# Kernel optimization log

Measured on AMD Instinct MI355X. Metric: run time of the kernel, lower is better.

## Reference

```python
import jax, jax.numpy as jnp
import numpy as np

DIM = 192
HEADS = 6
WH, WW = 7, 7
N = WH * WW            # 49 tokens per window
NW = 64                # windows per image
B = 64                 # images
B_ = NW * B            # 4096 window-batches
HEAD_DIM = DIM // HEADS
TABLE = (2 * WH - 1) * (2 * WW - 1)  # 169


def _relative_position_index():
    ch, cw = np.meshgrid(np.arange(WH), np.arange(WW), indexing='ij')
    coords = np.stack([ch, cw]).reshape(2, -1)          # (2, N)
    rel = coords[:, :, None] - coords[:, None, :]       # (2, N, N)
    rel = rel.transpose(1, 2, 0).astype(np.int32)
    rel[:, :, 0] += WH - 1
    rel[:, :, 1] += WW - 1
    rel[:, :, 0] *= 2 * WW - 1
    return jnp.asarray(rel.sum(-1))                     # (N, N) int32


def setup_inputs() -> dict:
    key = jax.random.key(0)
    ks = jax.random.split(key, 7)
    x = jax.random.normal(ks[0], (B_, N, DIM), dtype=jnp.float32)
    # 0 / -100 additive window mask (as produced by shifted-window masking)
    m = jax.random.uniform(ks[1], (NW, N, N))
    mask = jnp.where(m < 0.8, 0.0, -100.0).astype(jnp.float32)
    qkv_w = jax.random.normal(ks[2], (3 * DIM, DIM), dtype=jnp.float32) * 0.02
    qkv_b = jnp.zeros((3 * DIM,), dtype=jnp.float32)
    proj_w = jax.random.normal(ks[3], (DIM, DIM), dtype=jnp.float32) * 0.02
    proj_b = jnp.zeros((DIM,), dtype=jnp.float32)
    rpb_table = jax.random.normal(ks[4], (TABLE, HEADS), dtype=jnp.float32) * 0.02
    rel_idx = _relative_position_index()
    return {"x": x, "mask": mask, "qkv_w": qkv_w, "qkv_b": qkv_b,
            "proj_w": proj_w, "proj_b": proj_b, "rpb_table": rpb_table,
            "rel_idx": rel_idx}


def reference(x, mask, qkv_w, qkv_b, proj_w, proj_b, rpb_table, rel_idx):
    Bw, n, c = x.shape
    scale = HEAD_DIM ** -0.5
    qkv = x @ qkv_w.T + qkv_b                                  # (B_, N, 3C)
    qkv = qkv.reshape(Bw, n, 3, HEADS, HEAD_DIM).transpose(2, 0, 3, 1, 4)
    q, k, v = qkv[0], qkv[1], qkv[2]                           # (B_, H, N, hd)
    attn = jnp.einsum('bhid,bhjd->bhij', q * scale, k)          # (B_, H, N, N)
    bias = rpb_table[rel_idx.reshape(-1)].reshape(n, n, HEADS)  # gather
    attn = attn + bias.transpose(2, 0, 1)[None]                 # (1, H, N, N)
    nW = mask.shape[0]
    attn = attn.reshape(Bw // nW, nW, HEADS, n, n) + mask[None, :, None]
    attn = attn.reshape(Bw, HEADS, n, n)
    attn = jax.nn.softmax(attn, axis=-1).astype(v.dtype)
    out = jnp.einsum('bhij,bhjd->bhid', attn, v)                # (B_, H, N, hd)
    out = out.transpose(0, 2, 1, 3).reshape(Bw, n, c)
    return out @ proj_w.T + proj_b
```

## Files before the change

### kernel.cpp

```cpp
#include <hip/hip_runtime.h>

typedef unsigned short u16;
typedef unsigned int   u32;
typedef _Float16 f16x8 __attribute__((ext_vector_type(8)));
typedef __fp16   hf2   __attribute__((ext_vector_type(2)));
typedef float    f32x4 __attribute__((ext_vector_type(4)));

#define NTOK 49
#define CDIM 192
#define NH   6
#define HD   32

#define QOFF   0
#define QSTR   200
#define KOFF   9800
#define VTOFF  19600
#define VTSTR  56
#define XOFF   30352
#define PSTR   72
#define ARENA_U16 40152

#define WS_WQ 0
#define WS_WP 110592
#define WS_BM 147456

static __device__ __forceinline__ u16 f2h(float f){ union{ _Float16 h; u16 u;} v; v.h=(_Float16)f; return v.u; }
static __device__ __forceinline__ u32 pk2(float a, float b){
    hf2 h = __builtin_amdgcn_cvt_pkrtz(a, b);
    return __builtin_bit_cast(u32, h);
}

__global__ void prep_weights(const float* __restrict__ qkv_w,
                             const float* __restrict__ proj_w,
                             u16* __restrict__ ws)
{
    const int idx = blockIdx.x*256 + threadIdx.x;
    if (idx < 110592) {
        const int fid = idx >> 9, r = idx & 511;
        const int lane = r >> 3, e = r & 7;
        const int t = fid/6, k6 = fid - 6*t;
        const int col = t*16 + (lane & 15);
        const int kk  = k6*32 + (lane >> 4)*8 + e;
        ws[WS_WQ + idx] = f2h(qkv_w[col*CDIM + kk]);
    } else if (idx < 147456) {
        const int j = idx - 110592;
        const int fid = j >> 9, r = j & 511;
        const int lane = r >> 3, e = r & 7;
        const int t = fid/6, k6 = fid - 6*t;
        const int col = t*16 + (lane & 15);
        const int kk  = k6*32 + (lane >> 4)*8 + e;
        ws[WS_WP + j] = f2h(proj_w[col*CDIM + kk]);
    }
}

__global__ void prep_bm(const float* __restrict__ mask,
                        const float* __restrict__ rpb,
                        const int*   __restrict__ rel,
                        u16* __restrict__ ws)
{
    const int idx = blockIdx.x*256 + threadIdx.x;
    if (idx >= 64*NH*256*16) return;
    const int r   = idx & 3;
    const int jt  = (idx >> 2) & 3;
    const int tid = (idx >> 4) & 255;
    const int rest = idx >> 12;
    const int h = rest % NH;
    const int w = rest / NH;
    const int i  = 16*(tid >> 6) + (tid & 15);
    const int lg = (tid >> 4) & 3;
    const int j  = jt*16 + 4*lg + r;
    float v;
    if (i >= NTOK)      v = 0.0f;
    else if (j >= NTOK) v = -1e30f;
    else v = rpb[rel[i*NTOK+j]*NH + h] + mask[((size_t)w*NTOK+i)*NTOK + j];
    ws[WS_BM + idx] = f2h(v);
}

#define LDFRAG(B, BASE, t) { const u16* _p = (BASE) + (size_t)(t)*3072 + lane*8;      \
    B[0]=*(const f16x8*)(_p);      B[1]=*(const f16x8*)(_p+512);                      \
    B[2]=*(const f16x8*)(_p+1024); B[3]=*(const f16x8*)(_p+1536);                     \
    B[4]=*(const f16x8*)(_p+2048); B[5]=*(const f16x8*)(_p+2560); }

#define QKV_STEP(s, CUR, NXT, PF) {                                                   \
    if (PF) LDFRAG(NXT, wq, t0+(s)+2);                                                \
    const int _t = t0+(s); const int _sec = _t/12; const int _cb = (_t - _sec*12)*16; \
    f32x4 _ac[4] = {};                                                                \
    if (_sec < 2) {       \
      const float4 _b4 = *(const float4*)&qkv_b[_t*16 + 4*lg];                        \
      _Pragma("unroll") for (int _k=0;_k<6;++_k)                                      \
        _Pragma("unroll") for (int _m=0;_m<4;++_m)                                    \
          _ac[_m] = __builtin_amdgcn_mfma_f32_16x16x32_f16(CUR[_k], A[_k][_m], _ac[_m],0,0,0); \
      const float _sc = (_sec==0) ? 0.17677669529663687f : 1.0f;                      \
      u16* _dst = (_sec==0) ? (arena+QOFF) : (arena+KOFF);                            \
      _Pragma("unroll") for (int _m=0;_m<4;++_m) {                                    \
        const int _tok = 16*_m + l15;                                                 \
        if (_tok < NTOK) {                                                            \
          uint2 _wd = make_uint2(pk2((_ac[_m][0]+_b4.x)*_sc, (_ac[_m][1]+_b4.y)*_sc), \
                                 pk2((_ac[_m][2]+_b4.z)*_sc, (_ac[_m][3]+_b4.w)*_sc));\
          *(uint2*)&_dst[_tok*QSTR + _cb + 4*lg] = _wd; } }                           \
    } else {               \
      const float _b1 = qkv_b[384 + _cb + l15];                                       \
      _Pragma("unroll") for (int _k=0;_k<6;++_k)                                      \
        _Pragma("unroll") for (int _m=0;_m<4;++_m)                                    \
          _ac[_m] = __builtin_amdgcn_mfma_f32_16x16x32_f16(A[_k][_m], CUR[_k], _ac[_m],0,0,0); \
      _Pragma("unroll") for (int _m=0;_m<4;++_m) {                                    \
        if (16*_m + 4*lg <= 48) {                                                     \
          uint2 _wd = make_uint2(pk2(_ac[_m][0]+_b1, _ac[_m][1]+_b1),                 \
                                 pk2(_ac[_m][2]+_b1, _ac[_m][3]+_b1));                \
          *(uint2*)&arena[VTOFF + (_cb + l15)*VTSTR + 16*_m + 4*lg] = _wd; } } } }

#define PROJ_STEP(s, CUR, NXT, PF) {                                                  \
    if (PF) LDFRAG(NXT, wp, p0+(s)+1);                                                \
    f32x4 _ac[4] = {};                                                                \
    _Pragma("unroll") for (int _k=0;_k<6;++_k)                                        \
      _Pragma("unroll") for (int _m=0;_m<4;++_m)                                      \
        _ac[_m] = __builtin_amdgcn_mfma_f32_16x16x32_f16(CUR[_k], PA[_k][_m], _ac[_m],0,0,0); \
    _Pragma("unroll") for (int _m=0;_m<4;++_m) {                                      \
      const int _tok = 16*_m + l15;                                                   \
      if (_tok < NTOK) {                                                              \
        float4 _o = make_float4(_ac[_m][0]+pb4[s].x, _ac[_m][1]+pb4[s].y,             \
                                _ac[_m][2]+pb4[s].z, _ac[_m][3]+pb4[s].w);            \
        *(float4*)&og[(size_t)_tok*CDIM + (p0+(s))*16 + 4*lg] = _o; } } }

__global__ __launch_bounds__(256, 2)
void winattn_core(const float* __restrict__ x,
                  const float* __restrict__ qkv_b,
                  const float* __restrict__ proj_b,
                  const u16* __restrict__ ws,
                  float* __restrict__ out)
{
    __shared__ __align__(16) u16 arena[ARENA_U16];
    const int b    = blockIdx.x;
    const int tid  = threadIdx.x;
    const int lane = tid & 63;
    const int wv   = tid >> 6;
    const int l15  = lane & 15;
    const int lg   = lane >> 4;
    const int win  = b & 63;

    {
        const float4* xg = (const float4*)(x + (size_t)b * (NTOK * CDIM));
        for (int i = tid; i < NTOK * CDIM / 4; i += 256) {
            const float4 v = xg[i];
            const int row = (i * 4) / CDIM, col = (i * 4) % CDIM;
            *(uint2*)&arena[XOFF + row * QSTR + col] =
                make_uint2(pk2(v.x, v.y), pk2(v.z, v.w));
        }
        for (int i = tid; i < CDIM * 7; i += 256)
            arena[VTOFF + (i / 7) * VTSTR + 49 + (i % 7)] = 0;
    }
    __syncthreads();

    const u16* wq = ws + WS_WQ;
    int arow[4];
    #pragma unroll
    for (int m = 0; m < 4; ++m) {
        const int r = 16*m + l15;
        arow[m] = (r < NTOK ? r : NTOK-1) * QSTR;
    }
    const int t0 = wv * 9;
    {
        f16x8 A[6][4];
        #pragma unroll
        for (int k6 = 0; k6 < 6; ++k6)
            #pragma unroll
            for (int m = 0; m < 4; ++m)
                A[k6][m] = *(const f16x8*)&arena[XOFF + arow[m] + k6*32 + 8*lg];
        f16x8 Ba[6], Bb[6], Bc[6];
        LDFRAG(Ba, wq, t0); LDFRAG(Bb, wq, t0+1);
        QKV_STEP(0, Ba, Bc, 1)
        QKV_STEP(1, Bb, Ba, 1)
        QKV_STEP(2, Bc, Bb, 1)
        QKV_STEP(3, Ba, Bc, 1)
        QKV_STEP(4, Bb, Ba, 1)
        QKV_STEP(5, Bc, Bb, 1)
        QKV_STEP(6, Ba, Bc, 1)
        QKV_STEP(7, Bb, Ba, 0)
        QKV_STEP(8, Bc, Bb, 0)
    }

    f16x8 bmf[6][2];
    {
        const u16* bmb = ws + WS_BM + (((size_t)win*NH)*256 + tid)*16;
        #pragma unroll
        for (int h = 0; h < NH; ++h) {
            bmf[h][0] = *(const f16x8*)(bmb + h*4096);
            bmf[h][1] = *(const f16x8*)(bmb + h*4096 + 8);
        }
    }
    __syncthreads();

    const int i0 = 16 * wv;
    const bool myok = (i0 + l15 < NTOK);
    const int myrow = myok ? i0 + l15 : NTOK-1;
    int krow[4];
    #pragma unroll
    for (int jt = 0; jt < 4; ++jt)
        krow[jt] = (jt*16 + l15 < NTOK ? jt*16 + l15 : NTOK-1) * QSTR;

    f16x8 Qf[6];
    #pragma unroll
    for (int h = 0; h < NH; ++h)
        Qf[h] = *(const f16x8*)&arena[QOFF + myrow*QSTR + h*HD + 8*lg];

    #pragma unroll
    for (int h = 0; h < NH; ++h) {
        u16* pp = arena + XOFF + wv*2336 + (h & 1)*1168;
        f32x4 pacc[4];
        #pragma unroll
        for (int jt = 0; jt < 4; ++jt) {
            const f16x8 Kf = *(const f16x8*)&arena[KOFF + krow[jt] + h*HD + 8*lg];
            f32x4 z = {};
            pacc[jt] = __builtin_amdgcn_mfma_f32_16x16x32_f16(Kf, Qf[h], z, 0, 0, 0);
        }
        float val[4][4];
        float mx = -3e38f;
        #pragma unroll
        for (int jt = 0; jt < 4; ++jt)
            #pragma unroll
            for (int r = 0; r < 4; ++r) {
                val[jt][r] = pacc[jt][r] + (float)bmf[h][jt>>1][(jt&1)*4 + r];
                mx = fmaxf(mx, val[jt][r]);
            }
        mx = fmaxf(mx, __shfl_xor(mx, 16));
        mx = fmaxf(mx, __shfl_xor(mx, 32));
        float s = 0.f;
        #pragma unroll
        for (int jt = 0; jt < 4; ++jt)
            #pragma unroll
            for (int r = 0; r < 4; ++r) {
                const float e = __expf(val[jt][r] - mx);
                val[jt][r] = e; s += e;
            }
        s += __shfl_xor(s, 16);
        s += __shfl_xor(s, 32);
        const float inv = 1.0f / s;
        #pragma unroll
        for (int jt = 0; jt < 4; ++jt)
            *(uint2*)&pp[l15*PSTR + jt*16 + 4*lg] =
                make_uint2(pk2(val[jt][0], val[jt][1]), pk2(val[jt][2], val[jt][3]));
        const f16x8 Pb0 = *(const f16x8*)&pp[l15*PSTR + 8*lg];
        const f16x8 Pb1 = *(const f16x8*)&pp[l15*PSTR + 32 + 8*lg];
        const int a1 = (32 + 8*lg <= 48) ? 32 + 8*lg : 48;
        #pragma unroll
        for (int nt = 0; nt < 2; ++nt) {
            const int vr = (h*HD + nt*16 + l15) * VTSTR;
            const f16x8 Va0 = *(const f16x8*)&arena[VTOFF + vr + 8*lg];
            const f16x8 Va1 = *(const f16x8*)&arena[VTOFF + vr + a1];
            f32x4 o = {};
            o = __builtin_amdgcn_mfma_f32_16x16x32_f16(Va0, Pb0, o, 0, 0, 0);
            o = __builtin_amdgcn_mfma_f32_16x16x32_f16(Va1, Pb1, o, 0, 0, 0);
            if (myok) {
                *(uint2*)&arena[QOFF + (i0+l15)*QSTR + h*HD + nt*16 + 4*lg] =
                    make_uint2(pk2(o[0]*inv, o[1]*inv), pk2(o[2]*inv, o[3]*inv));
            }
        }
    }

    const u16* wp = ws + WS_WP;
    const int p0 = wv * 3;
    f16x8 Pa[6], Pb2[6];
    LDFRAG(Pa, wp, p0);
    float4 pb4[3];
    #pragma unroll
    for (int s = 0; s < 3; ++s)
        pb4[s] = *(const float4*)&proj_b[(p0+s)*16 + 4*lg];
    __syncthreads();
    {
        f16x8 PA[6][4];
        #pragma unroll
        for (int k6 = 0; k6 < 6; ++k6)
            #pragma unroll
            for (int m = 0; m < 4; ++m)
                PA[k6][m] = *(const f16x8*)&arena[QOFF + arow[m] + k6*32 + 8*lg];
        float* og = out + (size_t)b * (NTOK * CDIM);
        PROJ_STEP(0, Pa, Pb2, 1)
        PROJ_STEP(1, Pb2, Pa, 1)
        PROJ_STEP(2, Pa, Pb2, 0)
    }
}

extern "C" void kernel_launch(void* const* d_in, const int* in_sizes, int n_in,
                              void* d_out, int out_size, void* d_ws, size_t ws_size,
                              hipStream_t stream) {
    const float* x      = (const float*)d_in[0];
    const float* mask   = (const float*)d_in[1];
    const float* qkv_w  = (const float*)d_in[2];
    const float* qkv_b  = (const float*)d_in[3];
    const float* proj_w = (const float*)d_in[4];
    const float* proj_b = (const float*)d_in[5];
    const float* rpb    = (const float*)d_in[6];
    const int*   rel    = (const int*)d_in[7];
    u16* ws = (u16*)d_ws;

    const int nwin = in_sizes[0] / (NTOK * CDIM);
    prep_weights<<<576, 256, 0, stream>>>(qkv_w, proj_w, ws);
    prep_bm<<<(64*NH*256*16 + 255)/256, 256, 0, stream>>>(mask, rpb, rel, ws);
    winattn_core<<<nwin, 256, 0, stream>>>(x, qkv_b, proj_b, ws, (float*)d_out);
}
```

Measured before the change: 188.1 us.

## Load x fragments directly from global, fold scale/bias into weights and accumulators

```diff
diff --git a/kernel.cpp b/kernel.cpp
--- a/kernel.cpp
+++ b/kernel.cpp
@@ -10,15 +10,16 @@
 #define CDIM 192
 #define NH   6
 #define HD   32
+#define SC   0.17677669529663687f
 
 #define QOFF   0
 #define QSTR   200
 #define KOFF   9800
 #define VTOFF  19600
 #define VTSTR  56
-#define XOFF   30352
+#define POFF   30352
 #define PSTR   72
-#define ARENA_U16 40152
+#define ARENA_U16 39568
 
 #define WS_WQ 0
 #define WS_WP 110592
@@ -41,7 +42,9 @@
         const int t = fid/6, k6 = fid - 6*t;
         const int col = t*16 + (lane & 15);
         const int kk  = k6*32 + (lane >> 4)*8 + e;
-        ws[WS_WQ + idx] = f2h(qkv_w[col*CDIM + kk]);
+        float w = qkv_w[col*CDIM + kk];
+        if (col < CDIM) w *= SC;
+        ws[WS_WQ + idx] = f2h(w);
     } else if (idx < 147456) {
         const int j = idx - 110592;
         const int fid = j >> 9, r = j & 511;
@@ -84,42 +87,47 @@
 #define QKV_STEP(s, CUR, NXT, PF) {                                                   \
     if (PF) LDFRAG(NXT, wq, t0+(s)+2);                                                \
     const int _t = t0+(s); const int _sec = _t/12; const int _cb = (_t - _sec*12)*16; \
-    f32x4 _ac[4] = {};                                                                \
+    f32x4 _ac[4];                                                                     \
     if (_sec < 2) {       \
-      const float4 _b4 = *(const float4*)&qkv_b[_t*16 + 4*lg];                        \
+      float4 _b4 = *(const float4*)&qkv_b[_t*16 + 4*lg];                              \
+      if (_sec == 0) { _b4.x*=SC; _b4.y*=SC; _b4.z*=SC; _b4.w*=SC; }                  \
+      const f32x4 _ini = {_b4.x, _b4.y, _b4.z, _b4.w};                                \
+      _ac[0]=_ini; _ac[1]=_ini; _ac[2]=_ini; _ac[3]=_ini;                             \
       _Pragma("unroll") for (int _k=0;_k<6;++_k)                                      \
         _Pragma("unroll") for (int _m=0;_m<4;++_m)                                    \
           _ac[_m] = __builtin_amdgcn_mfma_f32_16x16x32_f16(CUR[_k], A[_k][_m], _ac[_m],0,0,0); \
-      const float _sc = (_sec==0) ? 0.17677669529663687f : 1.0f;                      \
       u16* _dst = (_sec==0) ? (arena+QOFF) : (arena+KOFF);                            \
       _Pragma("unroll") for (int _m=0;_m<4;++_m) {                                    \
         const int _tok = 16*_m + l15;                                                 \
         if (_tok < NTOK) {                                                            \
-          uint2 _wd = make_uint2(pk2((_ac[_m][0]+_b4.x)*_sc, (_ac[_m][1]+_b4.y)*_sc), \
-                                 pk2((_ac[_m][2]+_b4.z)*_sc, (_ac[_m][3]+_b4.w)*_sc));\
+          uint2 _wd = make_uint2(pk2(_ac[_m][0], _ac[_m][1]),                         \
+                                 pk2(_ac[_m][2], _ac[_m][3]));                        \
           *(uint2*)&_dst[_tok*QSTR + _cb + 4*lg] = _wd; } }                           \
-    } else {               \
+    } else {                            \
       const float _b1 = qkv_b[384 + _cb + l15];                                       \
+      const f32x4 _ini = {_b1, _b1, _b1, _b1};                                        \
+      _ac[0]=_ini; _ac[1]=_ini; _ac[2]=_ini; _ac[3]=_ini;                             \
       _Pragma("unroll") for (int _k=0;_k<6;++_k)                                      \
         _Pragma("unroll") for (int _m=0;_m<4;++_m)                                    \
           _ac[_m] = __builtin_amdgcn_mfma_f32_16x16x32_f16(A[_k][_m], CUR[_k], _ac[_m],0,0,0); \
       _Pragma("unroll") for (int _m=0;_m<4;++_m) {                                    \
         if (16*_m + 4*lg <= 48) {                                                     \
-          uint2 _wd = make_uint2(pk2(_ac[_m][0]+_b1, _ac[_m][1]+_b1),                 \
-                                 pk2(_ac[_m][2]+_b1, _ac[_m][3]+_b1));                \
+          uint2 _wd = make_uint2(pk2(_ac[_m][0], _ac[_m][1]),                         \
+                                 pk2(_ac[_m][2], _ac[_m][3]));                        \
           *(uint2*)&arena[VTOFF + (_cb + l15)*VTSTR + 16*_m + 4*lg] = _wd; } } } }
 
 #define PROJ_STEP(s, CUR, NXT, PF) {                                                  \
     if (PF) LDFRAG(NXT, wp, p0+(s)+1);                                                \
-    f32x4 _ac[4] = {};                                                                \
+    const f32x4 _ini = {pb4[s].x, pb4[s].y, pb4[s].z, pb4[s].w};                      \
+    f32x4 _ac[4];                                                                     \
+    _ac[0]=_ini; _ac[1]=_ini; _ac[2]=_ini; _ac[3]=_ini;                               \
     _Pragma("unroll") for (int _k=0;_k<6;++_k)                                        \
       _Pragma("unroll") for (int _m=0;_m<4;++_m)                                      \
         _ac[_m] = __builtin_amdgcn_mfma_f32_16x16x32_f16(CUR[_k], PA[_k][_m], _ac[_m],0,0,0); \
     _Pragma("unroll") for (int _m=0;_m<4;++_m) {                                      \
       const int _tok = 16*_m + l15;                                                   \
       if (_tok < NTOK) {                                                              \
-        float4 _o = make_float4(_ac[_m][0]+pb4[s].x, _ac[_m][1]+pb4[s].y,             \
-                                _ac[_m][2]+pb4[s].z, _ac[_m][3]+pb4[s].w);            \
+        float4 _o = make_float4(_ac[_m][0], _ac[_m][1], _ac[_m][2], _ac[_m][3]);      \
         *(float4*)&og[(size_t)_tok*CDIM + (p0+(s))*16 + 4*lg] = _o; } } }
 
 __global__ __launch_bounds__(256, 2)
@@ -138,34 +146,30 @@
     const int lg   = lane >> 4;
     const int win  = b & 63;
 
+    for (int i = tid; i < CDIM * 4; i += 256)
+        arena[VTOFF + (i >> 2) * VTSTR + 52 + (i & 3)] = 0;
+
+    f16x8 A[6][4];
     {
-        const float4* xg = (const float4*)(x + (size_t)b * (NTOK * CDIM));
-        for (int i = tid; i < NTOK * CDIM / 4; i += 256) {
-            const float4 v = xg[i];
-            const int row = (i * 4) / CDIM, col = (i * 4) % CDIM;
-            *(uint2*)&arena[XOFF + row * QSTR + col] =
-                make_uint2(pk2(v.x, v.y), pk2(v.z, v.w));
-        }
-        for (int i = tid; i < CDIM * 7; i += 256)
-            arena[VTOFF + (i / 7) * VTSTR + 49 + (i % 7)] = 0;
-    }
-    __syncthreads();
+        const float* xb = x + (size_t)b * (NTOK * CDIM);
+        #pragma unroll
+        for (int m = 0; m < 4; ++m) {
+            const int r = 16*m + l15;
+            const float* xr = xb + (size_t)(r < NTOK ? r : NTOK-1) * CDIM;
+            #pragma unroll
+            for (int k6 = 0; k6 < 6; ++k6) {
+                const float4 f0 = *(const float4*)&xr[k6*32 + 8*lg];
+                const float4 f1 = *(const float4*)&xr[k6*32 + 8*lg + 4];
+                const uint4 u = make_uint4(pk2(f0.x,f0.y), pk2(f0.z,f0.w),
+                                           pk2(f1.x,f1.y), pk2(f1.z,f1.w));
+                A[k6][m] = __builtin_bit_cast(f16x8, u);
+            }
+        }
+    }
 
     const u16* wq = ws + WS_WQ;
-    int arow[4];
-    #pragma unroll
-    for (int m = 0; m < 4; ++m) {
-        const int r = 16*m + l15;
-        arow[m] = (r < NTOK ? r : NTOK-1) * QSTR;
-    }
     const int t0 = wv * 9;
     {
-        f16x8 A[6][4];
-        #pragma unroll
-        for (int k6 = 0; k6 < 6; ++k6)
-            #pragma unroll
-            for (int m = 0; m < 4; ++m)
-                A[k6][m] = *(const f16x8*)&arena[XOFF + arow[m] + k6*32 + 8*lg];
         f16x8 Ba[6], Bb[6], Bc[6];
         LDFRAG(Ba, wq, t0); LDFRAG(Bb, wq, t0+1);
         QKV_STEP(0, Ba, Bc, 1)
@@ -203,56 +207,92 @@
     for (int h = 0; h < NH; ++h)
         Qf[h] = *(const f16x8*)&arena[QOFF + myrow*QSTR + h*HD + 8*lg];
 
-    #pragma unroll
-    for (int h = 0; h < NH; ++h) {
-        u16* pp = arena + XOFF + wv*2336 + (h & 1)*1168;
-        f32x4 pacc[4];
+    u16* pp0 = arena + POFF + wv*2304;
+    u16* pp1 = pp0 + 1152;
+
+    #pragma unroll
+    for (int hp = 0; hp < 3; ++hp) {
+        const int h0 = 2*hp, h1 = 2*hp + 1;
+        f32x4 pa0[4], pa1[4];
         #pragma unroll
         for (int jt = 0; jt < 4; ++jt) {
-            const f16x8 Kf = *(const f16x8*)&arena[KOFF + krow[jt] + h*HD + 8*lg];
+            const f16x8 Kf = *(const f16x8*)&arena[KOFF + krow[jt] + h0*HD + 8*lg];
             f32x4 z = {};
-            pacc[jt] = __builtin_amdgcn_mfma_f32_16x16x32_f16(Kf, Qf[h], z, 0, 0, 0);
-        }
-        float val[4][4];
-        float mx = -3e38f;
-        #pragma unroll
-        for (int jt = 0; jt < 4; ++jt)
-            #pragma unroll
-            for (int r = 0; r < 4; ++r) {
-                val[jt][r] = pacc[jt][r] + (float)bmf[h][jt>>1][(jt&1)*4 + r];
-                mx = fmaxf(mx, val[jt][r]);
-            }
-        mx = fmaxf(mx, __shfl_xor(mx, 16));
-        mx = fmaxf(mx, __shfl_xor(mx, 32));
-        float s = 0.f;
-        #pragma unroll
-        for (int jt = 0; jt < 4; ++jt)
-            #pragma unroll
-            for (int r = 0; r < 4; ++r) {
-                const float e = __expf(val[jt][r] - mx);
-                val[jt][r] = e; s += e;
-            }
-        s += __shfl_xor(s, 16);
-        s += __shfl_xor(s, 32);
-        const float inv = 1.0f / s;
-        #pragma unroll
-        for (int jt = 0; jt < 4; ++jt)
-            *(uint2*)&pp[l15*PSTR + jt*16 + 4*lg] =
-                make_uint2(pk2(val[jt][0], val[jt][1]), pk2(val[jt][2], val[jt][3]));
-        const f16x8 Pb0 = *(const f16x8*)&pp[l15*PSTR + 8*lg];
-        const f16x8 Pb1 = *(const f16x8*)&pp[l15*PSTR + 32 + 8*lg];
+            pa0[jt] = __builtin_amdgcn_mfma_f32_16x16x32_f16(Kf, Qf[h0], z, 0, 0, 0);
+        }
+        #pragma unroll
+        for (int jt = 0; jt < 4; ++jt) {
+            const f16x8 Kf = *(const f16x8*)&arena[KOFF + krow[jt] + h1*HD + 8*lg];
+            f32x4 z = {};
+            pa1[jt] = __builtin_amdgcn_mfma_f32_16x16x32_f16(Kf, Qf[h1], z, 0, 0, 0);
+        }
+        float inv0, inv1;
+        {
+            float val[4][4]; float mx = -3e38f;
+            #pragma unroll
+            for (int jt = 0; jt < 4; ++jt)
+                #pragma unroll
+                for (int r = 0; r < 4; ++r) {
+                    val[jt][r] = pa0[jt][r] + (float)bmf[h0][jt>>1][(jt&1)*4 + r];
+                    mx = fmaxf(mx, val[jt][r]);
+                }
+            mx = fmaxf(mx, __shfl_xor(mx, 16));
+            mx = fmaxf(mx, __shfl_xor(mx, 32));
+            float s = 0.f;
+            #pragma unroll
+            for (int jt = 0; jt < 4; ++jt)
+                #pragma unroll
+                for (int r = 0; r < 4; ++r) { const float e = __expf(val[jt][r]-mx); val[jt][r]=e; s+=e; }
+            s += __shfl_xor(s, 16); s += __shfl_xor(s, 32);
+            inv0 = 1.0f / s;
+            #pragma unroll
+            for (int jt = 0; jt < 4; ++jt)
+                *(uint2*)&pp0[l15*PSTR + jt*16 + 4*lg] =
+                    make_uint2(pk2(val[jt][0], val[jt][1]), pk2(val[jt][2], val[jt][3]));
+        }
+        {
+            float val[4][4]; float mx = -3e38f;
+            #pragma unroll
+            for (int jt = 0; jt < 4; ++jt)
+                #pragma unroll
+                for (int r = 0; r < 4; ++r) {
+                    val[jt][r] = pa1[jt][r] + (float)bmf[h1][jt>>1][(jt&1)*4 + r];
+                    mx = fmaxf(mx, val[jt][r]);
+                }
+            mx = fmaxf(mx, __shfl_xor(mx, 16));
+            mx = fmaxf(mx, __shfl_xor(mx, 32));
+            float s = 0.f;
+            #pragma unroll
+            for (int jt = 0; jt < 4; ++jt)
+                #pragma unroll
+                for (int r = 0; r < 4; ++r) { const float e = __expf(val[jt][r]-mx); val[jt][r]=e; s+=e; }
+            s += __shfl_xor(s, 16); s += __shfl_xor(s, 32);
+            inv1 = 1.0f / s;
+            #pragma unroll
+            for (int jt = 0; jt < 4; ++jt)
+                *(uint2*)&pp1[l15*PSTR + jt*16 + 4*lg] =
+                    make_uint2(pk2(val[jt][0], val[jt][1]), pk2(val[jt][2], val[jt][3]));
+        }
         const int a1 = (32 + 8*lg <= 48) ? 32 + 8*lg : 48;
         #pragma unroll
-        for (int nt = 0; nt < 2; ++nt) {
-            const int vr = (h*HD + nt*16 + l15) * VTSTR;
-            const f16x8 Va0 = *(const f16x8*)&arena[VTOFF + vr + 8*lg];
-            const f16x8 Va1 = *(const f16x8*)&arena[VTOFF + vr + a1];
-            f32x4 o = {};
-            o = __builtin_amdgcn_mfma_f32_16x16x32_f16(Va0, Pb0, o, 0, 0, 0);
-            o = __builtin_amdgcn_mfma_f32_16x16x32_f16(Va1, Pb1, o, 0, 0, 0);
-            if (myok) {
-                *(uint2*)&arena[QOFF + (i0+l15)*QSTR + h*HD + nt*16 + 4*lg] =
-                    make_uint2(pk2(o[0]*inv, o[1]*inv), pk2(o[2]*inv, o[3]*inv));
+        for (int e = 0; e < 2; ++e) {
+            const int h = e ? h1 : h0;
+            const u16* pp = e ? pp1 : pp0;
+            const float inv = e ? inv1 : inv0;
+            const f16x8 Pb0 = *(const f16x8*)&pp[l15*PSTR + 8*lg];
+            const f16x8 Pb1 = *(const f16x8*)&pp[l15*PSTR + 32 + 8*lg];
+            #pragma unroll
+            for (int nt = 0; nt < 2; ++nt) {
+                const int vr = (h*HD + nt*16 + l15) * VTSTR;
+                const f16x8 Va0 = *(const f16x8*)&arena[VTOFF + vr + 8*lg];
+                const f16x8 Va1 = *(const f16x8*)&arena[VTOFF + vr + a1];
+                f32x4 o = {};
+                o = __builtin_amdgcn_mfma_f32_16x16x32_f16(Va0, Pb0, o, 0, 0, 0);
+                o = __builtin_amdgcn_mfma_f32_16x16x32_f16(Va1, Pb1, o, 0, 0, 0);
+                if (myok) {
+                    *(uint2*)&arena[QOFF + (i0+l15)*QSTR + h*HD + nt*16 + 4*lg] =
+                        make_uint2(pk2(o[0]*inv, o[1]*inv), pk2(o[2]*inv, o[3]*inv));
+                }
             }
         }
     }
@@ -265,6 +305,12 @@
     #pragma unroll
     for (int s = 0; s < 3; ++s)
         pb4[s] = *(const float4*)&proj_b[(p0+s)*16 + 4*lg];
+    int arow[4];
+    #pragma unroll
+    for (int m = 0; m < 4; ++m) {
+        const int r = 16*m + l15;
+        arow[m] = (r < NTOK ? r : NTOK-1) * QSTR;
+    }
     __syncthreads();
     {
         f16x8 PA[6][4];
```

Measured after the change: 221.1 us. +17.5%, slower.

## Split window attention across 8 waves by token and head groups

Applied to the files above, without the earlier changes.

```diff
diff --git a/kernel.cpp b/kernel.cpp
--- a/kernel.cpp
+++ b/kernel.cpp
@@ -10,13 +10,14 @@
 #define CDIM 192
 #define NH   6
 #define HD   32
+#define SC   0.17677669529663687f
 
 #define QOFF   0
 #define QSTR   200
 #define KOFF   9800
 #define VTOFF  19600
 #define VTSTR  56
-#define XOFF   30352
+#define POFF   30352
 #define PSTR   72
 #define ARENA_U16 40152
 
@@ -41,7 +42,9 @@
         const int t = fid/6, k6 = fid - 6*t;
         const int col = t*16 + (lane & 15);
         const int kk  = k6*32 + (lane >> 4)*8 + e;
-        ws[WS_WQ + idx] = f2h(qkv_w[col*CDIM + kk]);
+        float w = qkv_w[col*CDIM + kk];
+        if (col < CDIM) w *= SC;
+        ws[WS_WQ + idx] = f2h(w);
     } else if (idx < 147456) {
         const int j = idx - 110592;
         const int fid = j >> 9, r = j & 511;
@@ -82,47 +85,52 @@
     B[4]=*(const f16x8*)(_p+2048); B[5]=*(const f16x8*)(_p+2560); }
 
 #define QKV_STEP(s, CUR, NXT, PF) {                                                   \
-    if (PF) LDFRAG(NXT, wq, t0+(s)+2);                                                \
+    if (PF) LDFRAG(NXT, wq, t0+(s)+1);                                                \
     const int _t = t0+(s); const int _sec = _t/12; const int _cb = (_t - _sec*12)*16; \
-    f32x4 _ac[4] = {};                                                                \
+    f32x4 _ac[2];                                                                     \
     if (_sec < 2) {       \
-      const float4 _b4 = *(const float4*)&qkv_b[_t*16 + 4*lg];                        \
+      float4 _b4 = *(const float4*)&qkv_b[_t*16 + 4*lg];                              \
+      if (_sec == 0) { _b4.x*=SC; _b4.y*=SC; _b4.z*=SC; _b4.w*=SC; }                  \
+      const f32x4 _ini = {_b4.x, _b4.y, _b4.z, _b4.w};                                \
+      _ac[0]=_ini; _ac[1]=_ini;                                                       \
       _Pragma("unroll") for (int _k=0;_k<6;++_k)                                      \
-        _Pragma("unroll") for (int _m=0;_m<4;++_m)                                    \
-          _ac[_m] = __builtin_amdgcn_mfma_f32_16x16x32_f16(CUR[_k], A[_k][_m], _ac[_m],0,0,0); \
-      const float _sc = (_sec==0) ? 0.17677669529663687f : 1.0f;                      \
+        _Pragma("unroll") for (int _mi=0;_mi<2;++_mi)                                 \
+          _ac[_mi] = __builtin_amdgcn_mfma_f32_16x16x32_f16(CUR[_k], A[_k][_mi], _ac[_mi],0,0,0); \
       u16* _dst = (_sec==0) ? (arena+QOFF) : (arena+KOFF);                            \
-      _Pragma("unroll") for (int _m=0;_m<4;++_m) {                                    \
-        const int _tok = 16*_m + l15;                                                 \
+      _Pragma("unroll") for (int _mi=0;_mi<2;++_mi) {                                 \
+        const int _tok = 32*mg + 16*_mi + l15;                                        \
         if (_tok < NTOK) {                                                            \
-          uint2 _wd = make_uint2(pk2((_ac[_m][0]+_b4.x)*_sc, (_ac[_m][1]+_b4.y)*_sc), \
-                                 pk2((_ac[_m][2]+_b4.z)*_sc, (_ac[_m][3]+_b4.w)*_sc));\
+          uint2 _wd = make_uint2(pk2(_ac[_mi][0], _ac[_mi][1]),                       \
+                                 pk2(_ac[_mi][2], _ac[_mi][3]));                      \
           *(uint2*)&_dst[_tok*QSTR + _cb + 4*lg] = _wd; } }                           \
-    } else {               \
+    } else {                            \
       const float _b1 = qkv_b[384 + _cb + l15];                                       \
+      const f32x4 _ini = {_b1, _b1, _b1, _b1};                                        \
+      _ac[0]=_ini; _ac[1]=_ini;                                                       \
       _Pragma("unroll") for (int _k=0;_k<6;++_k)                                      \
-        _Pragma("unroll") for (int _m=0;_m<4;++_m)                                    \
-          _ac[_m] = __builtin_amdgcn_mfma_f32_16x16x32_f16(A[_k][_m], CUR[_k], _ac[_m],0,0,0); \
-      _Pragma("unroll") for (int _m=0;_m<4;++_m) {                                    \
-        if (16*_m + 4*lg <= 48) {                                                     \
-          uint2 _wd = make_uint2(pk2(_ac[_m][0]+_b1, _ac[_m][1]+_b1),                 \
-                                 pk2(_ac[_m][2]+_b1, _ac[_m][3]+_b1));                \
-          *(uint2*)&arena[VTOFF + (_cb + l15)*VTSTR + 16*_m + 4*lg] = _wd; } } } }
+        _Pragma("unroll") for (int _mi=0;_mi<2;++_mi)                                 \
+          _ac[_mi] = __builtin_amdgcn_mfma_f32_16x16x32_f16(A[_k][_mi], CUR[_k], _ac[_mi],0,0,0); \
+      _Pragma("unroll") for (int _mi=0;_mi<2;++_mi) {                                 \
+        const int _tb = 32*mg + 16*_mi + 4*lg;                                        \
+        if (_tb <= 48) {                                                              \
+          uint2 _wd = make_uint2(pk2(_ac[_mi][0], _ac[_mi][1]),                       \
+                                 pk2(_ac[_mi][2], _ac[_mi][3]));                      \
+          *(uint2*)&arena[VTOFF + (_cb + l15)*VTSTR + _tb] = _wd; } } } }
 
 #define PROJ_STEP(s, CUR, NXT, PF) {                                                  \
     if (PF) LDFRAG(NXT, wp, p0+(s)+1);                                                \
-    f32x4 _ac[4] = {};                                                                \
+    const f32x4 _ini = {pb4[s].x, pb4[s].y, pb4[s].z, pb4[s].w};                      \
+    f32x4 _ac[2]; _ac[0]=_ini; _ac[1]=_ini;                                           \
     _Pragma("unroll") for (int _k=0;_k<6;++_k)                                        \
-      _Pragma("unroll") for (int _m=0;_m<4;++_m)                                      \
-        _ac[_m] = __builtin_amdgcn_mfma_f32_16x16x32_f16(CUR[_k], PA[_k][_m], _ac[_m],0,0,0); \
-    _Pragma("unroll") for (int _m=0;_m<4;++_m) {                                      \
-      const int _tok = 16*_m + l15;                                                   \
+      _Pragma("unroll") for (int _mi=0;_mi<2;++_mi)                                   \
+        _ac[_mi] = __builtin_amdgcn_mfma_f32_16x16x32_f16(CUR[_k], PA[_k][_mi], _ac[_mi],0,0,0); \
+    _Pragma("unroll") for (int _mi=0;_mi<2;++_mi) {                                   \
+      const int _tok = 32*mg + 16*_mi + l15;                                          \
       if (_tok < NTOK) {                                                              \
-        float4 _o = make_float4(_ac[_m][0]+pb4[s].x, _ac[_m][1]+pb4[s].y,             \
-                                _ac[_m][2]+pb4[s].z, _ac[_m][3]+pb4[s].w);            \
+        float4 _o = make_float4(_ac[_mi][0], _ac[_mi][1], _ac[_mi][2], _ac[_mi][3]);  \
         *(float4*)&og[(size_t)_tok*CDIM + (p0+(s))*16 + 4*lg] = _o; } } }
 
-__global__ __launch_bounds__(256, 2)
+__global__ __launch_bounds__(512, 4)
 void winattn_core(const float* __restrict__ x,
                   const float* __restrict__ qkv_b,
                   const float* __restrict__ proj_b,
@@ -134,63 +142,62 @@
     const int tid  = threadIdx.x;
     const int lane = tid & 63;
     const int wv   = tid >> 6;
+    const int rg   = wv & 3;
+    const int mg   = wv >> 2;
     const int l15  = lane & 15;
     const int lg   = lane >> 4;
     const int win  = b & 63;
 
     {
         const float4* xg = (const float4*)(x + (size_t)b * (NTOK * CDIM));
-        for (int i = tid; i < NTOK * CDIM / 4; i += 256) {
+        for (int i = tid; i < NTOK * CDIM / 4; i += 512) {
             const float4 v = xg[i];
             const int row = (i * 4) / CDIM, col = (i * 4) % CDIM;
-            *(uint2*)&arena[XOFF + row * QSTR + col] =
+            *(uint2*)&arena[POFF + row * QSTR + col] =
                 make_uint2(pk2(v.x, v.y), pk2(v.z, v.w));
         }
-        for (int i = tid; i < CDIM * 7; i += 256)
-            arena[VTOFF + (i / 7) * VTSTR + 49 + (i % 7)] = 0;
+        for (int i = tid; i < CDIM * 4; i += 512)
+            arena[VTOFF + (i >> 2) * VTSTR + 52 + (i & 3)] = 0;
     }
     __syncthreads();
 
     const u16* wq = ws + WS_WQ;
-    int arow[4];
-    #pragma unroll
-    for (int m = 0; m < 4; ++m) {
-        const int r = 16*m + l15;
-        arow[m] = (r < NTOK ? r : NTOK-1) * QSTR;
-    }
-    const int t0 = wv * 9;
+    const int t0 = rg * 9;
     {
-        f16x8 A[6][4];
-        #pragma unroll
-        for (int k6 = 0; k6 < 6; ++k6)
+        f16x8 A[6][2];
+        #pragma unroll
+        for (int mi = 0; mi < 2; ++mi) {
+            const int r = 32*mg + 16*mi + l15;
+            const int ar = (r < NTOK ? r : NTOK-1) * QSTR;
             #pragma unroll
-            for (int m = 0; m < 4; ++m)
-                A[k6][m] = *(const f16x8*)&arena[XOFF + arow[m] + k6*32 + 8*lg];
-        f16x8 Ba[6], Bb[6], Bc[6];
-        LDFRAG(Ba, wq, t0); LDFRAG(Bb, wq, t0+1);
-        QKV_STEP(0, Ba, Bc, 1)
+            for (int k6 = 0; k6 < 6; ++k6)
+                A[k6][mi] = *(const f16x8*)&arena[POFF + ar + k6*32 + 8*lg];
+        }
+        f16x8 Ba[6], Bb[6];
+        LDFRAG(Ba, wq, t0);
+        QKV_STEP(0, Ba, Bb, 1)
         QKV_STEP(1, Bb, Ba, 1)
-        QKV_STEP(2, Bc, Bb, 1)
-        QKV_STEP(3, Ba, Bc, 1)
-        QKV_STEP(4, Bb, Ba, 1)
-        QKV_STEP(5, Bc, Bb, 1)
-        QKV_STEP(6, Ba, Bc, 1)
-        QKV_STEP(7, Bb, Ba, 0)
-        QKV_STEP(8, Bc, Bb, 0)
-    }
-
-    f16x8 bmf[6][2];
+        QKV_STEP(2, Ba, Bb, 1)
+        QKV_STEP(3, Bb, Ba, 1)
+        QKV_STEP(4, Ba, Bb, 1)
+        QKV_STEP(5, Bb, Ba, 1)
+        QKV_STEP(6, Ba, Bb, 1)
+        QKV_STEP(7, Bb, Ba, 1)
+        QKV_STEP(8, Ba, Bb, 0)
+    }
+
+    f16x8 bmf[3][2];
     {
-        const u16* bmb = ws + WS_BM + (((size_t)win*NH)*256 + tid)*16;
-        #pragma unroll
-        for (int h = 0; h < NH; ++h) {
-            bmf[h][0] = *(const f16x8*)(bmb + h*4096);
-            bmf[h][1] = *(const f16x8*)(bmb + h*4096 + 8);
+        const u16* bmb = ws + WS_BM + ((((size_t)win*NH + 3*mg)*256) + rg*64 + lane)*16;
+        #pragma unroll
+        for (int h3 = 0; h3 < 3; ++h3) {
+            bmf[h3][0] = *(const f16x8*)(bmb + h3*4096);
+            bmf[h3][1] = *(const f16x8*)(bmb + h3*4096 + 8);
         }
     }
     __syncthreads();
 
-    const int i0 = 16 * wv;
+    const int i0 = 16 * rg;
     const bool myok = (i0 + l15 < NTOK);
     const int myrow = myok ? i0 + l15 : NTOK-1;
     int krow[4];
@@ -198,28 +205,30 @@
     for (int jt = 0; jt < 4; ++jt)
         krow[jt] = (jt*16 + l15 < NTOK ? jt*16 + l15 : NTOK-1) * QSTR;
 
-    f16x8 Qf[6];
+    f16x8 Qf[3];
     #pragma unroll
-    for (int h = 0; h < NH; ++h)
-        Qf[h] = *(const f16x8*)&arena[QOFF + myrow*QSTR + h*HD + 8*lg];
+    for (int h3 = 0; h3 < 3; ++h3)
+        Qf[h3] = *(const f16x8*)&arena[QOFF + myrow*QSTR + (3*mg+h3)*HD + 8*lg];
+
+    u16* pp = arena + POFF + wv*1152;
+    const int a1 = (32 + 8*lg <= 48) ? 32 + 8*lg : 48;
 
     #pragma unroll
-    for (int h = 0; h < NH; ++h) {
-        u16* pp = arena + XOFF + wv*2336 + (h & 1)*1168;
+    for (int h3 = 0; h3 < 3; ++h3) {
+        const int h = 3*mg + h3;
         f32x4 pacc[4];
         #pragma unroll
         for (int jt = 0; jt < 4; ++jt) {
             const f16x8 Kf = *(const f16x8*)&arena[KOFF + krow[jt] + h*HD + 8*lg];
             f32x4 z = {};
-            pacc[jt] = __builtin_amdgcn_mfma_f32_16x16x32_f16(Kf, Qf[h], z, 0, 0, 0);
-        }
-        float val[4][4];
-        float mx = -3e38f;
+            pacc[jt] = __builtin_amdgcn_mfma_f32_16x16x32_f16(Kf, Qf[h3], z, 0, 0, 0);
+        }
+        float val[4][4]; float mx = -3e38f;
         #pragma unroll
         for (int jt = 0; jt < 4; ++jt)
             #pragma unroll
             for (int r = 0; r < 4; ++r) {
-                val[jt][r] = pacc[jt][r] + (float)bmf[h][jt>>1][(jt&1)*4 + r];
+                val[jt][r] = pacc[jt][r] + (float)bmf[h3][jt>>1][(jt&1)*4 + r];
                 mx = fmaxf(mx, val[jt][r]);
             }
         mx = fmaxf(mx, __shfl_xor(mx, 16));
@@ -228,12 +237,8 @@
         #pragma unroll
         for (int jt = 0; jt < 4; ++jt)
             #pragma unroll
-            for (int r = 0; r < 4; ++r) {
-                const float e = __expf(val[jt][r] - mx);
-                val[jt][r] = e; s += e;
-            }
-        s += __shfl_xor(s, 16);
-        s += __shfl_xor(s, 32);
+            for (int r = 0; r < 4; ++r) { const float e = __expf(val[jt][r]-mx); val[jt][r]=e; s+=e; }
+        s += __shfl_xor(s, 16); s += __shfl_xor(s, 32);
         const float inv = 1.0f / s;
         #pragma unroll
         for (int jt = 0; jt < 4; ++jt)
@@ -241,7 +246,6 @@
                 make_uint2(pk2(val[jt][0], val[jt][1]), pk2(val[jt][2], val[jt][3]));
         const f16x8 Pb0 = *(const f16x8*)&pp[l15*PSTR + 8*lg];
         const f16x8 Pb1 = *(const f16x8*)&pp[l15*PSTR + 32 + 8*lg];
-        const int a1 = (32 + 8*lg <= 48) ? 32 + 8*lg : 48;
         #pragma unroll
         for (int nt = 0; nt < 2; ++nt) {
             const int vr = (h*HD + nt*16 + l15) * VTSTR;
@@ -258,7 +262,7 @@
     }
 
     const u16* wp = ws + WS_WP;
-    const int p0 = wv * 3;
+    const int p0 = rg * 3;
     f16x8 Pa[6], Pb2[6];
     LDFRAG(Pa, wp, p0);
     float4 pb4[3];
@@ -267,12 +271,15 @@
         pb4[s] = *(const float4*)&proj_b[(p0+s)*16 + 4*lg];
     __syncthreads();
     {
-        f16x8 PA[6][4];
-        #pragma unroll
-        for (int k6 = 0; k6 < 6; ++k6)
+        f16x8 PA[6][2];
+        #pragma unroll
+        for (int mi = 0; mi < 2; ++mi) {
+            const int r = 32*mg + 16*mi + l15;
+            const int ar = (r < NTOK ? r : NTOK-1) * QSTR;
             #pragma unroll
-            for (int m = 0; m < 4; ++m)
-                PA[k6][m] = *(const f16x8*)&arena[QOFF + arow[m] + k6*32 + 8*lg];
+            for (int k6 = 0; k6 < 6; ++k6)
+                PA[k6][mi] = *(const f16x8*)&arena[QOFF + ar + k6*32 + 8*lg];
+        }
         float* og = out + (size_t)b * (NTOK * CDIM);
         PROJ_STEP(0, Pa, Pb2, 1)
         PROJ_STEP(1, Pb2, Pa, 1)
@@ -296,5 +303,5 @@
     const int nwin = in_sizes[0] / (NTOK * CDIM);
     prep_weights<<<576, 256, 0, stream>>>(qkv_w, proj_w, ws);
     prep_bm<<<(64*NH*256*16 + 255)/256, 256, 0, stream>>>(mask, rpb, rel, ws);
-    winattn_core<<<nwin, 256, 0, stream>>>(x, qkv_b, proj_b, ws, (float*)d_out);
-}
+    winattn_core<<<nwin, 512, 0, stream>>>(x, qkv_b, proj_b, ws, (float*)d_out);
+}
```

After: 185.1 us. Within noise of the previous version (-1.6%).

## Stage x via direct global-to-LDS loads, fold scale/log2e into weights, bias-initialized accumulators

Applied to the files above, without the earlier changes.

```diff
diff --git a/kernel.cpp b/kernel.cpp
--- a/kernel.cpp
+++ b/kernel.cpp
@@ -10,13 +10,15 @@
 #define CDIM 192
 #define NH   6
 #define HD   32
+#define SC   0.17677669529663687f
+#define LOG2E 1.4426950408889634f
 
 #define QOFF   0
 #define QSTR   200
 #define KOFF   9800
 #define VTOFF  19600
 #define VTSTR  56
-#define XOFF   30352
+#define POFF   30352
 #define PSTR   72
 #define ARENA_U16 40152
 
@@ -28,6 +30,11 @@
 static __device__ __forceinline__ u32 pk2(float a, float b){
     hf2 h = __builtin_amdgcn_cvt_pkrtz(a, b);
     return __builtin_bit_cast(u32, h);
+}
+static __device__ __forceinline__ void gload16(const float* g, u16* l){
+    __builtin_amdgcn_global_load_lds(
+        (const __attribute__((address_space(1))) unsigned int*)g,
+        (__attribute__((address_space(3))) unsigned int*)l, 16, 0, 0);
 }
 
 __global__ void prep_weights(const float* __restrict__ qkv_w,
@@ -41,7 +48,9 @@
         const int t = fid/6, k6 = fid - 6*t;
         const int col = t*16 + (lane & 15);
         const int kk  = k6*32 + (lane >> 4)*8 + e;
-        ws[WS_WQ + idx] = f2h(qkv_w[col*CDIM + kk]);
+        float w = qkv_w[col*CDIM + kk];
+        if (col < CDIM) w *= SC * LOG2E;
+        ws[WS_WQ + idx] = f2h(w);
     } else if (idx < 147456) {
         const int j = idx - 110592;
         const int fid = j >> 9, r = j & 511;
@@ -72,7 +81,7 @@
     float v;
     if (i >= NTOK)      v = 0.0f;
     else if (j >= NTOK) v = -1e30f;
-    else v = rpb[rel[i*NTOK+j]*NH + h] + mask[((size_t)w*NTOK+i)*NTOK + j];
+    else v = (rpb[rel[i*NTOK+j]*NH + h] + mask[((size_t)w*NTOK+i)*NTOK + j]) * LOG2E;
     ws[WS_BM + idx] = f2h(v);
 }
 
@@ -82,44 +91,48 @@
     B[4]=*(const f16x8*)(_p+2048); B[5]=*(const f16x8*)(_p+2560); }
 
 #define QKV_STEP(s, CUR, NXT, PF) {                                                   \
-    if (PF) LDFRAG(NXT, wq, t0+(s)+2);                                                \
+    if (PF) { LDFRAG(NXT, wq, t0+(s)+2); }                                            \
     const int _t = t0+(s); const int _sec = _t/12; const int _cb = (_t - _sec*12)*16; \
-    f32x4 _ac[4] = {};                                                                \
+    f32x4 _ac[4];                                                                     \
     if (_sec < 2) {       \
-      const float4 _b4 = *(const float4*)&qkv_b[_t*16 + 4*lg];                        \
+      float4 _b4 = *(const float4*)&qkv_b[_t*16 + 4*lg];                              \
+      if (_sec == 0) { _b4.x*=SC*LOG2E; _b4.y*=SC*LOG2E; _b4.z*=SC*LOG2E; _b4.w*=SC*LOG2E; } \
+      const f32x4 _ini = {_b4.x, _b4.y, _b4.z, _b4.w};                                \
+      _ac[0]=_ini; _ac[1]=_ini; _ac[2]=_ini; _ac[3]=_ini;                             \
       _Pragma("unroll") for (int _k=0;_k<6;++_k)                                      \
         _Pragma("unroll") for (int _m=0;_m<4;++_m)                                    \
           _ac[_m] = __builtin_amdgcn_mfma_f32_16x16x32_f16(CUR[_k], A[_k][_m], _ac[_m],0,0,0); \
-      const float _sc = (_sec==0) ? 0.17677669529663687f : 1.0f;                      \
       u16* _dst = (_sec==0) ? (arena+QOFF) : (arena+KOFF);                            \
       _Pragma("unroll") for (int _m=0;_m<4;++_m) {                                    \
         const int _tok = 16*_m + l15;                                                 \
         if (_tok < NTOK) {                                                            \
-          uint2 _wd = make_uint2(pk2((_ac[_m][0]+_b4.x)*_sc, (_ac[_m][1]+_b4.y)*_sc), \
-                                 pk2((_ac[_m][2]+_b4.z)*_sc, (_ac[_m][3]+_b4.w)*_sc));\
+          uint2 _wd = make_uint2(pk2(_ac[_m][0], _ac[_m][1]),                         \
+                                 pk2(_ac[_m][2], _ac[_m][3]));                        \
           *(uint2*)&_dst[_tok*QSTR + _cb + 4*lg] = _wd; } }                           \
-    } else {               \
+    } else {                            \
       const float _b1 = qkv_b[384 + _cb + l15];                                       \
+      const f32x4 _ini = {_b1, _b1, _b1, _b1};                                        \
+      _ac[0]=_ini; _ac[1]=_ini; _ac[2]=_ini; _ac[3]=_ini;                             \
       _Pragma("unroll") for (int _k=0;_k<6;++_k)                                      \
         _Pragma("unroll") for (int _m=0;_m<4;++_m)                                    \
           _ac[_m] = __builtin_amdgcn_mfma_f32_16x16x32_f16(A[_k][_m], CUR[_k], _ac[_m],0,0,0); \
       _Pragma("unroll") for (int _m=0;_m<4;++_m) {                                    \
         if (16*_m + 4*lg <= 48) {                                                     \
-          uint2 _wd = make_uint2(pk2(_ac[_m][0]+_b1, _ac[_m][1]+_b1),                 \
-                                 pk2(_ac[_m][2]+_b1, _ac[_m][3]+_b1));                \
+          uint2 _wd = make_uint2(pk2(_ac[_m][0], _ac[_m][1]),                         \
+                                 pk2(_ac[_m][2], _ac[_m][3]));                        \
           *(uint2*)&arena[VTOFF + (_cb + l15)*VTSTR + 16*_m + 4*lg] = _wd; } } } }
 
 #define PROJ_STEP(s, CUR, NXT, PF) {                                                  \
-    if (PF) LDFRAG(NXT, wp, p0+(s)+1);                                                \
-    f32x4 _ac[4] = {};                                                                \
+    if (PF) { LDFRAG(NXT, wp, p0+(s)+1); }                                            \
+    const f32x4 _ini = {pb4[s].x, pb4[s].y, pb4[s].z, pb4[s].w};                      \
+    f32x4 _ac[4]; _ac[0]=_ini; _ac[1]=_ini; _ac[2]=_ini; _ac[3]=_ini;                 \
     _Pragma("unroll") for (int _k=0;_k<6;++_k)                                        \
       _Pragma("unroll") for (int _m=0;_m<4;++_m)                                      \
         _ac[_m] = __builtin_amdgcn_mfma_f32_16x16x32_f16(CUR[_k], PA[_k][_m], _ac[_m],0,0,0); \
     _Pragma("unroll") for (int _m=0;_m<4;++_m) {                                      \
       const int _tok = 16*_m + l15;                                                   \
       if (_tok < NTOK) {                                                              \
-        float4 _o = make_float4(_ac[_m][0]+pb4[s].x, _ac[_m][1]+pb4[s].y,             \
-                                _ac[_m][2]+pb4[s].z, _ac[_m][3]+pb4[s].w);            \
+        float4 _o = make_float4(_ac[_m][0], _ac[_m][1], _ac[_m][2], _ac[_m][3]);      \
         *(float4*)&og[(size_t)_tok*CDIM + (p0+(s))*16 + 4*lg] = _o; } } }
 
 __global__ __launch_bounds__(256, 2)
@@ -138,46 +151,56 @@
     const int lg   = lane >> 4;
     const int win  = b & 63;
 
+    const u16* wq = ws + WS_WQ;
+    const int t0 = wv * 9;
+
+    f16x8 Ba[6], Bb[6], Bc[6];
+    LDFRAG(Ba, wq, t0); LDFRAG(Bb, wq, t0+1);
+
     {
-        const float4* xg = (const float4*)(x + (size_t)b * (NTOK * CDIM));
-        for (int i = tid; i < NTOK * CDIM / 4; i += 256) {
-            const float4 v = xg[i];
-            const int row = (i * 4) / CDIM, col = (i * 4) % CDIM;
-            *(uint2*)&arena[XOFF + row * QSTR + col] =
-                make_uint2(pk2(v.x, v.y), pk2(v.z, v.w));
-        }
-        for (int i = tid; i < CDIM * 7; i += 256)
-            arena[VTOFF + (i / 7) * VTSTR + 49 + (i % 7)] = 0;
+        const float* xb = x + (size_t)b * (NTOK * CDIM);
+        for (int i = wv; i < 37; i += 4) {
+            const int p = i*64 + lane;
+            if (p < 2352) {
+                const int r = p / 48;
+                const int c = p - r*48;
+                const int g = r*48 + (c ^ (r & 7));
+                gload16(xb + g*4, &arena[i*512]);
+            }
+        }
+        for (int i = tid; i < CDIM * 4; i += 256)
+            arena[VTOFF + (i >> 2) * VTSTR + 52 + (i & 3)] = 0;
     }
     __syncthreads();
 
-    const u16* wq = ws + WS_WQ;
-    int arow[4];
+    f16x8 A[6][4];
     #pragma unroll
     for (int m = 0; m < 4; ++m) {
-        const int r = 16*m + l15;
-        arow[m] = (r < NTOK ? r : NTOK-1) * QSTR;
-    }
-    const int t0 = wv * 9;
-    {
-        f16x8 A[6][4];
-        #pragma unroll
-        for (int k6 = 0; k6 < 6; ++k6)
-            #pragma unroll
-            for (int m = 0; m < 4; ++m)
-                A[k6][m] = *(const f16x8*)&arena[XOFF + arow[m] + k6*32 + 8*lg];
-        f16x8 Ba[6], Bb[6], Bc[6];
-        LDFRAG(Ba, wq, t0); LDFRAG(Bb, wq, t0+1);
-        QKV_STEP(0, Ba, Bc, 1)
-        QKV_STEP(1, Bb, Ba, 1)
-        QKV_STEP(2, Bc, Bb, 1)
-        QKV_STEP(3, Ba, Bc, 1)
-        QKV_STEP(4, Bb, Ba, 1)
-        QKV_STEP(5, Bc, Bb, 1)
-        QKV_STEP(6, Ba, Bc, 1)
-        QKV_STEP(7, Bb, Ba, 0)
-        QKV_STEP(8, Bc, Bb, 0)
-    }
+        const int rr0 = 16*m + l15;
+        const int rr = rr0 < NTOK ? rr0 : NTOK-1;
+        const int sxr = rr & 7;
+        const int gb = rr * 48;
+        #pragma unroll
+        for (int k6 = 0; k6 < 6; ++k6) {
+            const int c0 = k6*8 + 2*lg;
+            const float4 f0 = *(const float4*)&arena[(gb + (c0 ^ sxr)) * 8];
+            const float4 f1 = *(const float4*)&arena[(gb + ((c0+1) ^ sxr)) * 8];
+            const uint4 u = make_uint4(pk2(f0.x,f0.y), pk2(f0.z,f0.w),
+                                       pk2(f1.x,f1.y), pk2(f1.z,f1.w));
+            A[k6][m] = __builtin_bit_cast(f16x8, u);
+        }
+    }
+    __syncthreads();
+
+    QKV_STEP(0, Ba, Bc, 1)
+    QKV_STEP(1, Bb, Ba, 1)
+    QKV_STEP(2, Bc, Bb, 1)
+    QKV_STEP(3, Ba, Bc, 1)
+    QKV_STEP(4, Bb, Ba, 1)
+    QKV_STEP(5, Bc, Bb, 1)
+    QKV_STEP(6, Ba, Bc, 1)
+    QKV_STEP(7, Bb, Ba, 0)
+    QKV_STEP(8, Bc, Bb, 0)
 
     f16x8 bmf[6][2];
     {
@@ -205,7 +228,7 @@
 
     #pragma unroll
     for (int h = 0; h < NH; ++h) {
-        u16* pp = arena + XOFF + wv*2336 + (h & 1)*1168;
+        u16* pp = arena + POFF + wv*2336 + (h & 1)*1168;
         f32x4 pacc[4];
         #pragma unroll
         for (int jt = 0; jt < 4; ++jt) {
@@ -229,7 +252,7 @@
         for (int jt = 0; jt < 4; ++jt)
             #pragma unroll
             for (int r = 0; r < 4; ++r) {
-                const float e = __expf(val[jt][r] - mx);
+                const float e = exp2f(val[jt][r] - mx);
                 val[jt][r] = e; s += e;
             }
         s += __shfl_xor(s, 16);
@@ -265,6 +288,12 @@
     #pragma unroll
     for (int s = 0; s < 3; ++s)
         pb4[s] = *(const float4*)&proj_b[(p0+s)*16 + 4*lg];
+    int arow[4];
+    #pragma unroll
+    for (int m = 0; m < 4; ++m) {
+        const int r = 16*m + l15;
+        arow[m] = (r < NTOK ? r : NTOK-1) * QSTR;
+    }
     __syncthreads();
     {
         f16x8 PA[6][4];
```

After: 173.4 us. -7.8%, faster.
